# Kernel optimization log

Measured on AMD Instinct MI355X. Metric: run time of the kernel, lower is better.

The kernel has to match this reference:

```python
import jax, jax.numpy as jnp
import numpy as np

NC = 50000
NG = 2000
D = 64
NE = 1000000
NP = 500000
BN_EPS = 1e-5


def setup_inputs() -> dict:
    key = jax.random.key(0)
    ks = jax.random.split(key, 16)
    return {
        "cell_feat1": jax.random.normal(ks[0], (NC, D), jnp.float32) * 0.05,
        "cell_feat2": jax.random.normal(ks[1], (NC, D), jnp.float32) * 0.05,
        "gene_feat": jax.random.normal(ks[2], (NG, D), jnp.float32) * 0.05,
        "emb_W": jax.random.normal(ks[3], (D + 2, D), jnp.float32) * 0.05,
        "emb_b": jnp.zeros((D,), jnp.float32),
        "bn_gamma": jnp.ones((D,), jnp.float32),
        "bn_beta": jnp.zeros((D,), jnp.float32),
        "bn_mean": jnp.zeros((D,), jnp.float32),
        "bn_var": jnp.ones((D,), jnp.float32),
        "enc_src1": jax.random.randint(ks[4], (NE,), 0, NC, jnp.int32),
        "enc_dst1": jax.random.randint(ks[5], (NE,), 0, NG, jnp.int32),
        "enc_src2": jax.random.randint(ks[6], (NE,), 0, NC, jnp.int32),
        "enc_dst2": jax.random.randint(ks[7], (NE,), 0, NG, jnp.int32),
        "pos_src1": jax.random.randint(ks[8], (NP,), 0, NC, jnp.int32),
        "pos_dst1": jax.random.randint(ks[9], (NP,), 0, NG, jnp.int32),
        "pos_src2": jax.random.randint(ks[10], (NP,), 0, NC, jnp.int32),
        "pos_dst2": jax.random.randint(ks[11], (NP,), 0, NG, jnp.int32),
    }


def _inv_sqrt_deg(idx, n):
    # deg^{-1/2} per node, 0 for isolated nodes; shape (n, 1)
    deg = jax.ops.segment_sum(jnp.ones_like(idx, jnp.float32), idx, num_segments=n)
    return jnp.where(deg > 0, jax.lax.rsqrt(jnp.maximum(deg, 1.0)), 0.0)[:, None]


def reference(cell_feat1, cell_feat2, gene_feat, emb_W, emb_b,
              bn_gamma, bn_beta, bn_mean, bn_var,
              enc_src1, enc_dst1, enc_src2, enc_dst2,
              pos_src1, pos_dst1, pos_src2, pos_dst2):
    nc, ng = cell_feat1.shape[0], gene_feat.shape[0]
    # degree normalizers per relation (cj = src deg^-1/2, ci = dst deg^-1/2)
    cj_c1 = _inv_sqrt_deg(enc_src1, nc)
    ci_g1 = _inv_sqrt_deg(enc_dst1, ng)
    cj_c2 = _inv_sqrt_deg(enc_src2, nc)
    ci_g2 = _inv_sqrt_deg(enc_dst2, ng)

    def spmm(src_feats, cj, src_idx, dst_idx, ci, n_dst):
        # gather-scale-scatter-scale: ci * sum_{j in N(i)} cj_j * h_j
        msgs = (src_feats * cj)[src_idx]
        return ci * jax.ops.segment_sum(msgs, dst_idx, num_segments=n_dst)

    def layer(c1, c2, g):
        # cell -> gene (two edge types, HeteroGraphConv aggregate='mean')
        g1 = spmm(c1, cj_c1, enc_src1, enc_dst1, ci_g1, ng)
        g2 = spmm(c2, cj_c2, enc_src2, enc_dst2, ci_g2, ng)
        g_new = 0.5 * (g1 + g2)
        # gene -> cell (reverse edges; roles of ci/cj swap)
        c1_new = spmm(g, ci_g1, enc_dst1, enc_src1, cj_c1, nc)
        c2_new = spmm(g, ci_g2, enc_dst2, enc_src2, cj_c2, nc)
        return c1_new, c2_new, g_new

    w = jnp.float32(1.0 / 3.0)  # n_layers == 2 -> weights [1/3, 1/3, 1/3]
    u1, u2, ih = w * cell_feat1, w * cell_feat2, w * gene_feat
    c1, c2, g = cell_feat1, cell_feat2, gene_feat
    for _ in range(2):
        c1, c2, g = layer(c1, c2, g)
        u1 = u1 + w * c1
        u2 = u2 + w * c2
        ih = ih + w * g

    # emb_layer: Linear(d+2 -> d) on [feat | batch one-hot], BN (eval), ELU
    def emb(u, onehot):
        x = jnp.concatenate([u, jnp.broadcast_to(onehot, (u.shape[0], 2))], axis=1)
        y = x @ emb_W + emb_b
        y = bn_gamma * (y - bn_mean) * jax.lax.rsqrt(bn_var + BN_EPS) + bn_beta
        return jax.nn.elu(y)

    uf1 = emb(u1, jnp.array([1.0, 0.0], jnp.float32))
    uf2 = emb(u2, jnp.array([0.0, 1.0], jnp.float32))

    # DotDecoder: per-positive-edge dot product
    pred1 = jnp.sum(uf1[pos_src1] * ih[pos_dst1], axis=1)
    pred2 = jnp.sum(uf2[pos_src2] * ih[pos_dst2], axis=1)
    return jnp.concatenate([pred1, pred2])
```

## Files before the change

kernel.cpp:

```cpp
#include <hip/hip_runtime.h>
#include <math.h>

#define NC   50000
#define NG   2000
#define DD   64
#define NE   1000000
#define NPOS 500000
#define WTH  (1.0f/3.0f)

#define GSTRIDE 640
#define CSTRIDE 64

#define NRNGB  256
#define RNGCB  196
#define RCAP   4608
#define NRNGG  250
#define GPRG   8
#define RCAPG  4608
#define CHUNKB 4096

typedef unsigned short u16;
typedef unsigned char  u8;

__device__ __forceinline__ float bf2f(u16 u) {
    return __uint_as_float(((unsigned)u) << 16);
}
__device__ __forceinline__ u16 f2bf(float f) {
    unsigned x = __float_as_uint(f);
    return (u16)((x + 0x7FFFu + ((x >> 16) & 1u)) >> 16);
}
__device__ __forceinline__ float blo(unsigned u) { return __uint_as_float(u << 16); }
__device__ __forceinline__ float bhi(unsigned u) { return __uint_as_float(u & 0xFFFF0000u); }
__device__ __forceinline__ float rdlane(float v, int l) {
    return __uint_as_float((unsigned)__builtin_amdgcn_readlane(__float_as_uint(v), l));
}

__global__ __launch_bounds__(256) void k_bin2(
    const int* __restrict__ s1, const int* __restrict__ d1,
    const int* __restrict__ s2, const int* __restrict__ d2,
    int* __restrict__ rcnt_c1, int* __restrict__ rcnt_c2,
    int* __restrict__ rcnt_g1, int* __restrict__ rcnt_g2,
    unsigned* __restrict__ rbc1, unsigned* __restrict__ rbc2,
    unsigned* __restrict__ rbg1, unsigned* __restrict__ rbg2)
{
    __shared__ unsigned ed[CHUNKB];
    __shared__ unsigned hc[NRNGB], bc[NRNGB];
    __shared__ unsigned hg[NRNGG], bg[NRNGG];
    const int* src; const int* dst; int* rc; int* rg; unsigned* rbc; unsigned* rbg;
    if (blockIdx.y == 0) { src = s1; dst = d1; rc = rcnt_c1; rg = rcnt_g1; rbc = rbc1; rbg = rbg1; }
    else                 { src = s2; dst = d2; rc = rcnt_c2; rg = rcnt_g2; rbc = rbc2; rbg = rbg2; }
    int t = threadIdx.x;
    if (t < NRNGB) hc[t] = 0;
    if (t < NRNGG) hg[t] = 0;
    __syncthreads();
    int e0 = blockIdx.x * CHUNKB;
    #pragma unroll 4
    for (int i = 0; i < CHUNKB / 256; i++) {
        int e = e0 + i * 256 + t;
        unsigned pk = 0xFFFFFFFFu;
        if (e < NE) {
            int s = src[e], g = dst[e];
            pk = ((unsigned)s << 16) | (unsigned)g;
            atomicAdd(&hc[s / RNGCB], 1u);
            atomicAdd(&hg[g >> 3], 1u);
        }
        ed[i * 256 + t] = pk;
    }
    __syncthreads();
    if (t < NRNGB) { unsigned c = hc[t]; bc[t] = c ? (unsigned)atomicAdd(&rc[t], (int)c) : 0u; hc[t] = 0; }
    if (t < NRNGG) { unsigned c = hg[t]; bg[t] = c ? (unsigned)atomicAdd(&rg[t], (int)c) : 0u; hg[t] = 0; }
    __syncthreads();
    #pragma unroll 4
    for (int i = 0; i < CHUNKB / 256; i++) {
        unsigned pk = ed[i * 256 + t];
        if (pk != 0xFFFFFFFFu) {
            int s = (int)(pk >> 16), g = (int)(pk & 0xFFFFu);
            int r1 = s / RNGCB;
            unsigned p = bc[r1] + atomicAdd(&hc[r1], 1u);
            if (p < RCAP)
                rbc[(size_t)r1 * RCAP + p] = ((unsigned)(s - r1 * RNGCB) << 16) | (unsigned)g;
            int r2 = g >> 3;
            unsigned q = bg[r2] + atomicAdd(&hg[r2], 1u);
            if (q < RCAPG)
                rbg[(size_t)r2 * RCAPG + q] = ((unsigned)(g & 7) << 16) | (unsigned)s;
        }
    }
}

__global__ __launch_bounds__(256) void k_binfill(
    const int* __restrict__ rcnt1, const int* __restrict__ rcnt2,
    const unsigned* __restrict__ rbuf1, const unsigned* __restrict__ rbuf2,
    unsigned* __restrict__ adj_c1, unsigned* __restrict__ adj_c2,
    int* __restrict__ cnt_c1, int* __restrict__ cnt_c2)
{
    __shared__ unsigned rows[RNGCB * CSTRIDE];
    __shared__ unsigned cur[(RNGCB + 3) / 4];
    const int* rcnt; const unsigned* rbuf; unsigned* adj; int* cnt;
    if (blockIdx.y == 0) { rcnt = rcnt1; rbuf = rbuf1; adj = adj_c1; cnt = cnt_c1; }
    else                 { rcnt = rcnt2; rbuf = rbuf2; adj = adj_c2; cnt = cnt_c2; }
    int t = threadIdx.x;
    int r = blockIdx.x;
    if (t < (RNGCB + 3) / 4) cur[t] = 0;
    __syncthreads();
    int n = rcnt[r]; if (n > RCAP) n = RCAP;
    const unsigned* buf = rbuf + (size_t)r * RCAP;
    for (int i = t; i < n; i += 256) {
        unsigned e = buf[i];
        unsigned cl = e >> 16;
        unsigned sh = 8u * (cl & 3u);
        unsigned old = atomicAdd(&cur[cl >> 2], 1u << sh);
        unsigned p = (old >> sh) & 0xFFu;
        if (p < CSTRIDE) rows[cl * CSTRIDE + p] = (e & 0xFFFFu) << 8;
    }
    __syncthreads();
    int lo = r * RNGCB;
    int valid = NC - lo; if (valid > RNGCB) valid = RNGCB;
    if (valid <= 0) return;
    if (t < valid) {
        unsigned p = (cur[t >> 2] >> (8u * (t & 3u))) & 0xFFu;
        cnt[lo + t] = (int)((p > CSTRIDE) ? CSTRIDE : p);
    }
    uint4* gd = (uint4*)(adj + (size_t)lo * CSTRIDE);
    const uint4* ls = (const uint4*)rows;
    for (int i = t; i < valid * (CSTRIDE / 4); i += 256) gd[i] = ls[i];
}

__global__ __launch_bounds__(256) void k_binfill_g(
    const int* __restrict__ rcnt1, const int* __restrict__ rcnt2,
    const unsigned* __restrict__ rbuf1, const unsigned* __restrict__ rbuf2,
    unsigned* __restrict__ adj_g1, unsigned* __restrict__ adj_g2,
    int* __restrict__ cnt_g1, int* __restrict__ cnt_g2)
{
    __shared__ unsigned rows[GPRG * GSTRIDE];
    __shared__ unsigned cur[GPRG];
    const int* rcnt; const unsigned* rbuf; unsigned* adj; int* cnt;
    if (blockIdx.y == 0) { rcnt = rcnt1; rbuf = rbuf1; adj = adj_g1; cnt = cnt_g1; }
    else                 { rcnt = rcnt2; rbuf = rbuf2; adj = adj_g2; cnt = cnt_g2; }
    int t = threadIdx.x;
    int r = blockIdx.x;
    if (t < GPRG) cur[t] = 0;
    __syncthreads();
    int n = rcnt[r]; if (n > RCAPG) n = RCAPG;
    const unsigned* buf = rbuf + (size_t)r * RCAPG;
    for (int i = t; i < n; i += 256) {
        unsigned e = buf[i];
        unsigned gl = e >> 16;
        unsigned p = atomicAdd(&cur[gl], 1u);
        if (p < GSTRIDE) rows[gl * GSTRIDE + p] = (e & 0xFFFFu) << 7;
    }
    __syncthreads();
    if (t < GPRG) {
        unsigned p = cur[t];
        cnt[r * GPRG + t] = (int)((p > GSTRIDE) ? GSTRIDE : p);
    }
    uint4* gd = (uint4*)(adj + (size_t)r * GPRG * GSTRIDE);
    const uint4* ls = (const uint4*)rows;
    for (int i = t; i < GPRG * GSTRIDE / 4; i += 256) gd[i] = ls[i];
}

__global__ __launch_bounds__(256) void k_prep(
    const int* __restrict__ cnt_c1, const int* __restrict__ cnt_c2,
    const int* __restrict__ cnt_g1, const int* __restrict__ cnt_g2,
    const float* __restrict__ cell1, const float* __restrict__ cell2,
    const float* __restrict__ gfeat,
    float* __restrict__ cj_c1, float* __restrict__ cj_c2,
    float* __restrict__ ci_g1, float* __restrict__ ci_g2,
    u16* __restrict__ t1s, u16* __restrict__ t2s,
    u16* __restrict__ gfb1, u16* __restrict__ gfb2)
{
    int i = blockIdx.x * 4 + (threadIdx.x >> 6);
    int d = threadIdx.x & 63;
    if (i < NC) {
        int a = cnt_c1[i]; float j1 = (a > 0) ? 1.0f / sqrtf((float)a) : 0.0f;
        int b = cnt_c2[i]; float j2 = (b > 0) ? 1.0f / sqrtf((float)b) : 0.0f;
        if (d == 0) { cj_c1[i] = j1; cj_c2[i] = j2; }
        int idx = i * DD + d;
        t1s[idx] = f2bf(cell1[idx] * j1);
        t2s[idx] = f2bf(cell2[idx] * j2);
    }
    if (i < NG) {
        int a = cnt_g1[i]; float j1 = (a > 0) ? 1.0f / sqrtf((float)a) : 0.0f;
        int b = cnt_g2[i]; float j2 = (b > 0) ? 1.0f / sqrtf((float)b) : 0.0f;
        if (d == 0) { ci_g1[i] = j1; ci_g2[i] = j2; }
        int idx = i * DD + d;
        float g = gfeat[idx];
        gfb1[2 * idx] = f2bf(g * j1);
        gfb2[2 * idx] = f2bf(g * j2);
    }
}

__global__ __launch_bounds__(256) void k_c2g(
    const u16* __restrict__ src1s, const u16* __restrict__ src2s,
    const unsigned* __restrict__ adj_g1, const int* __restrict__ cnt_g1,
    const unsigned* __restrict__ adj_g2, const int* __restrict__ cnt_g2,
    const float* __restrict__ ci_g1, const float* __restrict__ ci_g2,
    u16* __restrict__ gb1s, u16* __restrict__ gb2s,
    const float* __restrict__ gfeat_init,
    float* __restrict__ ih, u16* __restrict__ ihb)
{
    __shared__ float l1[4][DD];
    __shared__ float l2[4][DD];
    int i   = blockIdx.x;
    int d   = threadIdx.x & 63;
    int grp = threadIdx.x >> 6;
    int d2b = 2 * d;
    const char* sb1 = (const char*)src1s;
    const char* sb2 = (const char*)src2s;

    int n1 = cnt_g1[i]; if (n1 > GSTRIDE) n1 = GSTRIDE;
    const unsigned* a1 = adj_g1 + (size_t)i * GSTRIDE;
    float acc1 = 0.f;
    int e = 0;
    for (; e + 32 <= n1; e += 32) {
        uint4 wa = *(const uint4*)(a1 + e + grp * 8);
        uint4 wb = *(const uint4*)(a1 + e + grp * 8 + 4);
        float v0 = bf2f(*(const u16*)(sb1 + wa.x + d2b)), v1 = bf2f(*(const u16*)(sb1 + wa.y + d2b));
        float v2 = bf2f(*(const u16*)(sb1 + wa.z + d2b)), v3 = bf2f(*(const u16*)(sb1 + wa.w + d2b));
        float v4 = bf2f(*(const u16*)(sb1 + wb.x + d2b)), v5 = bf2f(*(const u16*)(sb1 + wb.y + d2b));
        float v6 = bf2f(*(const u16*)(sb1 + wb.z + d2b)), v7 = bf2f(*(const u16*)(sb1 + wb.w + d2b));
        acc1 += ((v0 + v1) + (v2 + v3)) + ((v4 + v5) + (v6 + v7));
    }
    for (int q = e + grp; q < n1; q += 4) acc1 += bf2f(*(const u16*)(sb1 + a1[q] + d2b));

    int n2 = cnt_g2[i]; if (n2 > GSTRIDE) n2 = GSTRIDE;
    const unsigned* a2 = adj_g2 + (size_t)i * GSTRIDE;
    float acc2 = 0.f;
    e = 0;
    for (; e + 32 <= n2; e += 32) {
        uint4 wa = *(const uint4*)(a2 + e + grp * 8);
        uint4 wb = *(const uint4*)(a2 + e + grp * 8 + 4);
        float v0 = bf2f(*(const u16*)(sb2 + wa.x + d2b)), v1 = bf2f(*(const u16*)(sb2 + wa.y + d2b));
        float v2 = bf2f(*(const u16*)(sb2 + wa.z + d2b)), v3 = bf2f(*(const u16*)(sb2 + wa.w + d2b));
        float v4 = bf2f(*(const u16*)(sb2 + wb.x + d2b)), v5 = bf2f(*(const u16*)(sb2 + wb.y + d2b));
        float v6 = bf2f(*(const u16*)(sb2 + wb.z + d2b)), v7 = bf2f(*(const u16*)(sb2 + wb.w + d2b));
        acc2 += ((v0 + v1) + (v2 + v3)) + ((v4 + v5) + (v6 + v7));
    }
    for (int q = e + grp; q < n2; q += 4) acc2 += bf2f(*(const u16*)(sb2 + a2[q] + d2b));

    l1[grp][d] = acc1; l2[grp][d] = acc2;
    __syncthreads();
    if (grp == 0) {
        float s1 = l1[0][d] + l1[1][d] + l1[2][d] + l1[3][d];
        float s2 = l2[0][d] + l2[1][d] + l2[2][d] + l2[3][d];
        float ci1 = ci_g1[i], ci2 = ci_g2[i];
        float gn = 0.5f * (ci1 * s1 + ci2 * s2);
        int idx = i * DD + d;
        if (gb1s) { gb1s[2 * idx + 1] = f2bf(gn * ci1); gb2s[2 * idx + 1] = f2bf(gn * ci2); }
        if (gfeat_init) ih[idx] = WTH * (gfeat_init[idx] + gn);
        else            ihb[idx] = f2bf(ih[idx] + WTH * gn);
    }
}

__global__ __launch_bounds__(256, 4) void k_g2c2_emb(
    const u16* __restrict__ gfb1, const u16* __restrict__ gfb2,
    const unsigned* __restrict__ adj_c1, const int* __restrict__ cnt_c1,
    const unsigned* __restrict__ adj_c2, const int* __restrict__ cnt_c2,
    const float* __restrict__ cj_c1, const float* __restrict__ cj_c2,
    const float* __restrict__ cell1, const float* __restrict__ cell2,
    u16* __restrict__ c1bs, u16* __restrict__ c2bs,
    u16* __restrict__ uf1b, u16* __restrict__ uf2b,
    const float* __restrict__ W, const float* __restrict__ bb,
    const float* __restrict__ gam, const float* __restrict__ bet,
    const float* __restrict__ mea, const float* __restrict__ var)
{
    int d = threadIdx.x & 63;
    int wid = blockIdx.x * 4 + (threadIdx.x >> 6);
    int nw = gridDim.x * 4;

    float Wl[DD];
    #pragma unroll
    for (int k = 0; k < DD; k++) Wl[k] = W[k * DD + d];
    float inv = 1.0f / sqrtf(var[d] + 1e-5f);
    float ga = gam[d], be = bet[d], me = mea[d];
    float bias1 = bb[d] + W[DD * DD + d];
    float bias2 = bb[d] + W[(DD + 1) * DD + d];
    int d4 = 4 * d;
    const char* gb1 = (const char*)gfb1;
    const char* gb2 = (const char*)gfb2;

    for (int i = wid; i < NC; i += nw) {
        int n1 = cnt_c1[i]; if (n1 > CSTRIDE) n1 = CSTRIDE;
        int n2 = cnt_c2[i]; if (n2 > CSTRIDE) n2 = CSTRIDE;
        const unsigned* a1 = adj_c1 + (size_t)i * CSTRIDE;
        const unsigned* a2 = adj_c2 + (size_t)i * CSTRIDE;
        float a1A = 0.f, a2A = 0.f;
        float a1B = 0.f, a2B = 0.f;
        int e1 = 0, e2 = 0;
        int m1 = n1 & ~3, m2 = n2 & ~3;
        int m = (m1 < m2) ? m1 : m2;
        for (; e1 < m; e1 += 4, e2 += 4) {
            uint4 w1 = *(const uint4*)(a1 + e1);
            uint4 w2 = *(const uint4*)(a2 + e2);
            unsigned p0 = *(const unsigned*)(gb1 + w1.x + d4);
            unsigned p1 = *(const unsigned*)(gb1 + w1.y + d4);
            unsigned p2 = *(const unsigned*)(gb1 + w1.z + d4);
            unsigned p3 = *(const unsigned*)(gb1 + w1.w + d4);
            unsigned q0 = *(const unsigned*)(gb2 + w2.x + d4);
            unsigned q1 = *(const unsigned*)(gb2 + w2.y + d4);
            unsigned q2 = *(const unsigned*)(gb2 + w2.z + d4);
            unsigned q3 = *(const unsigned*)(gb2 + w2.w + d4);
            a1A += (blo(p0) + blo(p1)) + (blo(p2) + blo(p3));
            a1B += (bhi(p0) + bhi(p1)) + (bhi(p2) + bhi(p3));
            a2A += (blo(q0) + blo(q1)) + (blo(q2) + blo(q3));
            a2B += (bhi(q0) + bhi(q1)) + (bhi(q2) + bhi(q3));
        }
        for (; e1 + 3 < n1; e1 += 4) {
            uint4 w1 = *(const uint4*)(a1 + e1);
            unsigned p0 = *(const unsigned*)(gb1 + w1.x + d4);
            unsigned p1 = *(const unsigned*)(gb1 + w1.y + d4);
            unsigned p2 = *(const unsigned*)(gb1 + w1.z + d4);
            unsigned p3 = *(const unsigned*)(gb1 + w1.w + d4);
            a1A += (blo(p0) + blo(p1)) + (blo(p2) + blo(p3));
            a1B += (bhi(p0) + bhi(p1)) + (bhi(p2) + bhi(p3));
        }
        for (; e1 < n1; e1++) {
            unsigned p = *(const unsigned*)(gb1 + a1[e1] + d4);
            a1A += blo(p); a1B += bhi(p);
        }
        for (; e2 + 3 < n2; e2 += 4) {
            uint4 w2 = *(const uint4*)(a2 + e2);
            unsigned q0 = *(const unsigned*)(gb2 + w2.x + d4);
            unsigned q1 = *(const unsigned*)(gb2 + w2.y + d4);
            unsigned q2 = *(const unsigned*)(gb2 + w2.z + d4);
            unsigned q3 = *(const unsigned*)(gb2 + w2.w + d4);
            a2A += (blo(q0) + blo(q1)) + (blo(q2) + blo(q3));
            a2B += (bhi(q0) + bhi(q1)) + (bhi(q2) + bhi(q3));
        }
        for (; e2 < n2; e2++) {
            unsigned q = *(const unsigned*)(gb2 + a2[e2] + d4);
            a2A += blo(q); a2B += bhi(q);
        }

        float jc1 = cj_c1[i], jc2 = cj_c2[i];
        float c1n = jc1 * a1A;
        float c2n = jc2 * a2A;
        int idx = i * DD + d;
        c1bs[idx] = f2bf(c1n * jc1);
        c2bs[idx] = f2bf(c2n * jc2);
        float x1 = WTH * (cell1[idx] + c1n) + WTH * (jc1 * a1B);
        float x2 = WTH * (cell2[idx] + c2n) + WTH * (jc2 * a2B);

        float y1 = bias1, y2 = bias2;
        #pragma unroll
        for (int k = 0; k < DD; k++) {
            float xa = rdlane(x1, k);
            float xb = rdlane(x2, k);
            y1 += xa * Wl[k];
            y2 += xb * Wl[k];
        }
        float t1 = ga * (y1 - me) * inv + be;
        t1 = (t1 > 0.f) ? t1 : expm1f(t1);
        float t2 = ga * (y2 - me) * inv + be;
        t2 = (t2 > 0.f) ? t2 : expm1f(t2);
        uf1b[idx] = f2bf(t1);
        uf2b[idx] = f2bf(t2);
    }
}

__global__ __launch_bounds__(256) void k_dec(
    const u16* __restrict__ uf1b, const u16* __restrict__ uf2b,
    const u16* __restrict__ ihb,
    const int* __restrict__ ps1, const int* __restrict__ pd1,
    const int* __restrict__ ps2, const int* __restrict__ pd2,
    float* __restrict__ out)
{
    int t = blockIdx.x * 256 + threadIdx.x;
    int e = t >> 3;
    int l = t & 7;
    if (e >= 2 * NPOS) return;
    const u16* uf; int s, g;
    if (e < NPOS) { uf = uf1b; s = ps1[e];        g = pd1[e];        }
    else          { uf = uf2b; s = ps2[e - NPOS]; g = pd2[e - NPOS]; }
    uint4 av = ((const uint4*)(uf + (size_t)s * DD))[l];
    uint4 cv = ((const uint4*)(ihb + (size_t)g * DD))[l];
    float acc = blo(av.x) * blo(cv.x) + bhi(av.x) * bhi(cv.x)
              + blo(av.y) * blo(cv.y) + bhi(av.y) * bhi(cv.y)
              + blo(av.z) * blo(cv.z) + bhi(av.z) * bhi(cv.z)
              + blo(av.w) * blo(cv.w) + bhi(av.w) * bhi(cv.w);
    acc += __shfl_xor(acc, 4);
    acc += __shfl_xor(acc, 2);
    acc += __shfl_xor(acc, 1);
    if (l == 0) out[e] = acc;
}

extern "C" void kernel_launch(void* const* d_in, const int* in_sizes, int n_in,
                              void* d_out, int out_size, void* d_ws, size_t ws_size,
                              hipStream_t stream)
{
    const float* cell1 = (const float*)d_in[0];
    const float* cell2 = (const float*)d_in[1];
    const float* gfeat = (const float*)d_in[2];
    const float* embW  = (const float*)d_in[3];
    const float* embB  = (const float*)d_in[4];
    const float* bng   = (const float*)d_in[5];
    const float* bnb   = (const float*)d_in[6];
    const float* bnm   = (const float*)d_in[7];
    const float* bnv   = (const float*)d_in[8];
    const int* es1 = (const int*)d_in[9];
    const int* ed1 = (const int*)d_in[10];
    const int* es2 = (const int*)d_in[11];
    const int* ed2 = (const int*)d_in[12];
    const int* ps1 = (const int*)d_in[13];
    const int* pd1 = (const int*)d_in[14];
    const int* ps2 = (const int*)d_in[15];
    const int* pd2 = (const int*)d_in[16];
    float* out = (float*)d_out;

    char* base = (char*)d_ws;
    size_t off = 0;
    auto alloc = [&](size_t bytes) -> void* {
        void* p = base + off;
        off = (off + bytes + 255) & ~(size_t)255;
        return p;
    };
    int* rcnt_c1 = (int*)alloc((size_t)NRNGB * 4);
    int* rcnt_c2 = (int*)alloc((size_t)NRNGB * 4);
    int* rcnt_g1 = (int*)alloc((size_t)NRNGG * 4);
    int* rcnt_g2 = (int*)alloc((size_t)NRNGG * 4);
    size_t cntEnd = off;
    int* cnt_c1 = (int*)alloc((size_t)NC * 4);
    int* cnt_c2 = (int*)alloc((size_t)NC * 4);
    int* cnt_g1 = (int*)alloc((size_t)NG * 4);
    int* cnt_g2 = (int*)alloc((size_t)NG * 4);
    unsigned* rbc1 = (unsigned*)alloc((size_t)NRNGB * RCAP * 4);
    unsigned* rbc2 = (unsigned*)alloc((size_t)NRNGB * RCAP * 4);
    unsigned* rbg1 = (unsigned*)alloc((size_t)NRNGG * RCAPG * 4);
    unsigned* rbg2 = (unsigned*)alloc((size_t)NRNGG * RCAPG * 4);
    unsigned* adj_c1 = (unsigned*)alloc((size_t)NC * CSTRIDE * 4);
    unsigned* adj_c2 = (unsigned*)alloc((size_t)NC * CSTRIDE * 4);
    unsigned* adj_g1 = (unsigned*)alloc((size_t)NG * GSTRIDE * 4);
    unsigned* adj_g2 = (unsigned*)alloc((size_t)NG * GSTRIDE * 4);
    float* cj_c1 = (float*)alloc((size_t)NC * 4);
    float* cj_c2 = (float*)alloc((size_t)NC * 4);
    float* ci_g1 = (float*)alloc((size_t)NG * 4);
    float* ci_g2 = (float*)alloc((size_t)NG * 4);
    u16* t1s  = (u16*)alloc((size_t)NC * DD * 2);
    u16* t2s  = (u16*)alloc((size_t)NC * DD * 2);
    u16* c1bs = (u16*)alloc((size_t)NC * DD * 2);
    u16* c2bs = (u16*)alloc((size_t)NC * DD * 2);
    u16* gfb1 = (u16*)alloc((size_t)NG * DD * 2 * 2);
    u16* gfb2 = (u16*)alloc((size_t)NG * DD * 2 * 2);
    float* ih  = (float*)alloc((size_t)NG * DD * 4);
    u16*   ihb = (u16*)alloc((size_t)NG * DD * 2);
    (void)ws_size; (void)in_sizes; (void)n_in; (void)out_size;

    hipMemsetAsync(d_ws, 0, cntEnd, stream);

    dim3 gr((NE + CHUNKB - 1) / CHUNKB, 2);
    k_bin2<<<gr, 256, 0, stream>>>(es1, ed1, es2, ed2,
                                   rcnt_c1, rcnt_c2, rcnt_g1, rcnt_g2,
                                   rbc1, rbc2, rbg1, rbg2);
    dim3 gf(NRNGB, 2);
    k_binfill<<<gf, 256, 0, stream>>>(rcnt_c1, rcnt_c2, rbc1, rbc2,
                                      adj_c1, adj_c2, cnt_c1, cnt_c2);
    dim3 gg(NRNGG, 2);
    k_binfill_g<<<gg, 256, 0, stream>>>(rcnt_g1, rcnt_g2, rbg1, rbg2,
                                        adj_g1, adj_g2, cnt_g1, cnt_g2);
    k_prep<<<(NC + 3) / 4, 256, 0, stream>>>(cnt_c1, cnt_c2, cnt_g1, cnt_g2,
                                             cell1, cell2, gfeat,
                                             cj_c1, cj_c2, ci_g1, ci_g2,
                                             t1s, t2s, gfb1, gfb2);

    k_c2g<<<NG, 256, 0, stream>>>(t1s, t2s, adj_g1, cnt_g1, adj_g2, cnt_g2,
                                  ci_g1, ci_g2, gfb1, gfb2, gfeat, ih, nullptr);
    k_g2c2_emb<<<2048, 256, 0, stream>>>(gfb1, gfb2,
                                         adj_c1, cnt_c1, adj_c2, cnt_c2,
                                         cj_c1, cj_c2, cell1, cell2,
                                         c1bs, c2bs, t1s, t2s,
                                         embW, embB, bng, bnb, bnm, bnv);
    k_c2g<<<NG, 256, 0, stream>>>(c1bs, c2bs, adj_g1, cnt_g1, adj_g2, cnt_g2,
                                  ci_g1, ci_g2, nullptr, nullptr, nullptr, ih, ihb);
    k_dec<<<(2 * NPOS * 8 + 255) / 256, 256, 0, stream>>>(t1s, t2s, ihb,
                                                          ps1, pd1, ps2, pd2, out);
}
```

Measured before the change: 359.0 us.

## Replace two-pass binned adjacency build with direct global-atomic scatter

Replaces the three-kernel binning pipeline (range histogram, bucket buffers, shared-memory fill) with a single kernel where each edge does global atomicAdd on per-node counters and writes directly into fixed-stride adjacency rows. This removes two launches and the intermediate bucket buffers with their extra read and write pass. The cost is heavy global atomic contention, especially on the 2000 gene counters, which receive about 500 edges each, plus scattered uncoalesced writes. Adjacency slot order is also no longer deterministic.

```diff
diff --git a/kernel.cpp b/kernel.cpp
--- a/kernel.cpp
+++ b/kernel.cpp
@@ -11,14 +11,6 @@
 #define GSTRIDE 640
 #define CSTRIDE 64
 
-#define NRNGB  256
-#define RNGCB  196
-#define RCAP   4608
-#define NRNGG  250
-#define GPRG   8
-#define RCAPG  4608
-#define CHUNKB 4096
-
 typedef unsigned short u16;
 typedef unsigned char  u8;
 
@@ -35,127 +27,24 @@
     return __uint_as_float((unsigned)__builtin_amdgcn_readlane(__float_as_uint(v), l));
 }
 
-__global__ __launch_bounds__(256) void k_bin2(
+__global__ __launch_bounds__(256) void k_build(
     const int* __restrict__ s1, const int* __restrict__ d1,
     const int* __restrict__ s2, const int* __restrict__ d2,
-    int* __restrict__ rcnt_c1, int* __restrict__ rcnt_c2,
-    int* __restrict__ rcnt_g1, int* __restrict__ rcnt_g2,
-    unsigned* __restrict__ rbc1, unsigned* __restrict__ rbc2,
-    unsigned* __restrict__ rbg1, unsigned* __restrict__ rbg2)
-{
-    __shared__ unsigned ed[CHUNKB];
-    __shared__ unsigned hc[NRNGB], bc[NRNGB];
-    __shared__ unsigned hg[NRNGG], bg[NRNGG];
-    const int* src; const int* dst; int* rc; int* rg; unsigned* rbc; unsigned* rbg;
-    if (blockIdx.y == 0) { src = s1; dst = d1; rc = rcnt_c1; rg = rcnt_g1; rbc = rbc1; rbg = rbg1; }
-    else                 { src = s2; dst = d2; rc = rcnt_c2; rg = rcnt_g2; rbc = rbc2; rbg = rbg2; }
-    int t = threadIdx.x;
-    if (t < NRNGB) hc[t] = 0;
-    if (t < NRNGG) hg[t] = 0;
-    __syncthreads();
-    int e0 = blockIdx.x * CHUNKB;
-    #pragma unroll 4
-    for (int i = 0; i < CHUNKB / 256; i++) {
-        int e = e0 + i * 256 + t;
-        unsigned pk = 0xFFFFFFFFu;
-        if (e < NE) {
-            int s = src[e], g = dst[e];
-            pk = ((unsigned)s << 16) | (unsigned)g;
-            atomicAdd(&hc[s / RNGCB], 1u);
-            atomicAdd(&hg[g >> 3], 1u);
-        }
-        ed[i * 256 + t] = pk;
-    }
-    __syncthreads();
-    if (t < NRNGB) { unsigned c = hc[t]; bc[t] = c ? (unsigned)atomicAdd(&rc[t], (int)c) : 0u; hc[t] = 0; }
-    if (t < NRNGG) { unsigned c = hg[t]; bg[t] = c ? (unsigned)atomicAdd(&rg[t], (int)c) : 0u; hg[t] = 0; }
-    __syncthreads();
-    #pragma unroll 4
-    for (int i = 0; i < CHUNKB / 256; i++) {
-        unsigned pk = ed[i * 256 + t];
-        if (pk != 0xFFFFFFFFu) {
-            int s = (int)(pk >> 16), g = (int)(pk & 0xFFFFu);
-            int r1 = s / RNGCB;
-            unsigned p = bc[r1] + atomicAdd(&hc[r1], 1u);
-            if (p < RCAP)
-                rbc[(size_t)r1 * RCAP + p] = ((unsigned)(s - r1 * RNGCB) << 16) | (unsigned)g;
-            int r2 = g >> 3;
-            unsigned q = bg[r2] + atomicAdd(&hg[r2], 1u);
-            if (q < RCAPG)
-                rbg[(size_t)r2 * RCAPG + q] = ((unsigned)(g & 7) << 16) | (unsigned)s;
-        }
-    }
-}
-
-__global__ __launch_bounds__(256) void k_binfill(
-    const int* __restrict__ rcnt1, const int* __restrict__ rcnt2,
-    const unsigned* __restrict__ rbuf1, const unsigned* __restrict__ rbuf2,
+    int* __restrict__ cnt_c1, int* __restrict__ cnt_c2,
+    int* __restrict__ cnt_g1, int* __restrict__ cnt_g2,
     unsigned* __restrict__ adj_c1, unsigned* __restrict__ adj_c2,
-    int* __restrict__ cnt_c1, int* __restrict__ cnt_c2)
-{
-    __shared__ unsigned rows[RNGCB * CSTRIDE];
-    __shared__ unsigned cur[(RNGCB + 3) / 4];
-    const int* rcnt; const unsigned* rbuf; unsigned* adj; int* cnt;
-    if (blockIdx.y == 0) { rcnt = rcnt1; rbuf = rbuf1; adj = adj_c1; cnt = cnt_c1; }
-    else                 { rcnt = rcnt2; rbuf = rbuf2; adj = adj_c2; cnt = cnt_c2; }
-    int t = threadIdx.x;
-    int r = blockIdx.x;
-    if (t < (RNGCB + 3) / 4) cur[t] = 0;
-    __syncthreads();
-    int n = rcnt[r]; if (n > RCAP) n = RCAP;
-    const unsigned* buf = rbuf + (size_t)r * RCAP;
-    for (int i = t; i < n; i += 256) {
-        unsigned e = buf[i];
-        unsigned cl = e >> 16;
-        unsigned sh = 8u * (cl & 3u);
-        unsigned old = atomicAdd(&cur[cl >> 2], 1u << sh);
-        unsigned p = (old >> sh) & 0xFFu;
-        if (p < CSTRIDE) rows[cl * CSTRIDE + p] = (e & 0xFFFFu) << 8;
-    }
-    __syncthreads();
-    int lo = r * RNGCB;
-    int valid = NC - lo; if (valid > RNGCB) valid = RNGCB;
-    if (valid <= 0) return;
-    if (t < valid) {
-        unsigned p = (cur[t >> 2] >> (8u * (t & 3u))) & 0xFFu;
-        cnt[lo + t] = (int)((p > CSTRIDE) ? CSTRIDE : p);
-    }
-    uint4* gd = (uint4*)(adj + (size_t)lo * CSTRIDE);
-    const uint4* ls = (const uint4*)rows;
-    for (int i = t; i < valid * (CSTRIDE / 4); i += 256) gd[i] = ls[i];
-}
-
-__global__ __launch_bounds__(256) void k_binfill_g(
-    const int* __restrict__ rcnt1, const int* __restrict__ rcnt2,
-    const unsigned* __restrict__ rbuf1, const unsigned* __restrict__ rbuf2,
-    unsigned* __restrict__ adj_g1, unsigned* __restrict__ adj_g2,
-    int* __restrict__ cnt_g1, int* __restrict__ cnt_g2)
-{
-    __shared__ unsigned rows[GPRG * GSTRIDE];
-    __shared__ unsigned cur[GPRG];
-    const int* rcnt; const unsigned* rbuf; unsigned* adj; int* cnt;
-    if (blockIdx.y == 0) { rcnt = rcnt1; rbuf = rbuf1; adj = adj_g1; cnt = cnt_g1; }
-    else                 { rcnt = rcnt2; rbuf = rbuf2; adj = adj_g2; cnt = cnt_g2; }
-    int t = threadIdx.x;
-    int r = blockIdx.x;
-    if (t < GPRG) cur[t] = 0;
-    __syncthreads();
-    int n = rcnt[r]; if (n > RCAPG) n = RCAPG;
-    const unsigned* buf = rbuf + (size_t)r * RCAPG;
-    for (int i = t; i < n; i += 256) {
-        unsigned e = buf[i];
-        unsigned gl = e >> 16;
-        unsigned p = atomicAdd(&cur[gl], 1u);
-        if (p < GSTRIDE) rows[gl * GSTRIDE + p] = (e & 0xFFFFu) << 7;
-    }
-    __syncthreads();
-    if (t < GPRG) {
-        unsigned p = cur[t];
-        cnt[r * GPRG + t] = (int)((p > GSTRIDE) ? GSTRIDE : p);
-    }
-    uint4* gd = (uint4*)(adj + (size_t)r * GPRG * GSTRIDE);
-    const uint4* ls = (const uint4*)rows;
-    for (int i = t; i < GPRG * GSTRIDE / 4; i += 256) gd[i] = ls[i];
+    unsigned* __restrict__ adj_g1, unsigned* __restrict__ adj_g2)
+{
+    const int* src; const int* dst; int* cc; int* cg; unsigned* ac; unsigned* ag;
+    if (blockIdx.y == 0) { src = s1; dst = d1; cc = cnt_c1; cg = cnt_g1; ac = adj_c1; ag = adj_g1; }
+    else                 { src = s2; dst = d2; cc = cnt_c2; cg = cnt_g2; ac = adj_c2; ag = adj_g2; }
+    int e = blockIdx.x * 256 + threadIdx.x;
+    if (e >= NE) return;
+    int s = src[e], g = dst[e];
+    int p = atomicAdd(&cc[s], 1);
+    if (p < CSTRIDE) ac[(size_t)s * CSTRIDE + p] = ((unsigned)g) << 8;
+    int q = atomicAdd(&cg[g], 1);
+    if (q < GSTRIDE) ag[(size_t)g * GSTRIDE + q] = ((unsigned)s) << 7;
 }
 
 __global__ __launch_bounds__(256) void k_prep(
@@ -413,19 +302,11 @@
         off = (off + bytes + 255) & ~(size_t)255;
         return p;
     };
-    int* rcnt_c1 = (int*)alloc((size_t)NRNGB * 4);
-    int* rcnt_c2 = (int*)alloc((size_t)NRNGB * 4);
-    int* rcnt_g1 = (int*)alloc((size_t)NRNGG * 4);
-    int* rcnt_g2 = (int*)alloc((size_t)NRNGG * 4);
-    size_t cntEnd = off;
     int* cnt_c1 = (int*)alloc((size_t)NC * 4);
     int* cnt_c2 = (int*)alloc((size_t)NC * 4);
     int* cnt_g1 = (int*)alloc((size_t)NG * 4);
     int* cnt_g2 = (int*)alloc((size_t)NG * 4);
-    unsigned* rbc1 = (unsigned*)alloc((size_t)NRNGB * RCAP * 4);
-    unsigned* rbc2 = (unsigned*)alloc((size_t)NRNGB * RCAP * 4);
-    unsigned* rbg1 = (unsigned*)alloc((size_t)NRNGG * RCAPG * 4);
-    unsigned* rbg2 = (unsigned*)alloc((size_t)NRNGG * RCAPG * 4);
+    size_t cntEnd = off;
     unsigned* adj_c1 = (unsigned*)alloc((size_t)NC * CSTRIDE * 4);
     unsigned* adj_c2 = (unsigned*)alloc((size_t)NC * CSTRIDE * 4);
     unsigned* adj_g1 = (unsigned*)alloc((size_t)NG * GSTRIDE * 4);
@@ -446,16 +327,10 @@
 
     hipMemsetAsync(d_ws, 0, cntEnd, stream);
 
-    dim3 gr((NE + CHUNKB - 1) / CHUNKB, 2);
-    k_bin2<<<gr, 256, 0, stream>>>(es1, ed1, es2, ed2,
-                                   rcnt_c1, rcnt_c2, rcnt_g1, rcnt_g2,
-                                   rbc1, rbc2, rbg1, rbg2);
-    dim3 gf(NRNGB, 2);
-    k_binfill<<<gf, 256, 0, stream>>>(rcnt_c1, rcnt_c2, rbc1, rbc2,
-                                      adj_c1, adj_c2, cnt_c1, cnt_c2);
-    dim3 gg(NRNGG, 2);
-    k_binfill_g<<<gg, 256, 0, stream>>>(rcnt_g1, rcnt_g2, rbg1, rbg2,
-                                        adj_g1, adj_g2, cnt_g1, cnt_g2);
+    dim3 gb((NE + 255) / 256, 2);
+    k_build<<<gb, 256, 0, stream>>>(es1, ed1, es2, ed2,
+                                    cnt_c1, cnt_c2, cnt_g1, cnt_g2,
+                                    adj_c1, adj_c2, adj_g1, adj_g2);
     k_prep<<<(NC + 3) / 4, 256, 0, stream>>>(cnt_c1, cnt_c2, cnt_g1, cnt_g2,
                                              cell1, cell2, gfeat,
                                              cj_c1, cj_c2, ci_g1, ci_g2,
```

Measured after the change: 606.2 us. +68.8%, slower.
